# Performance work log

Hardware: AMD Instinct MI355X
Metric: run time of the kernel (lower is better)

Reference implementation:

```python
import jax, jax.numpy as jnp
import numpy as np

N_NODES = 50000
N_EDGES = 800000
IN_CH = 128
HID = 64
HEADS = 4
OUT_CH = 64
NEG_SLOPE = 0.2
EPS = 1e-16


def setup_inputs() -> dict:
    key = jax.random.key(0)
    ks = jax.random.split(key, 12)
    x = jax.random.normal(ks[0], (N_NODES, IN_CH), dtype=jnp.float32)
    edge_index = jax.random.randint(ks[1], (2, N_EDGES), 0, N_NODES, dtype=jnp.int32)
    s1 = 1.0 / np.sqrt(IN_CH)
    s2 = 1.0 / np.sqrt(HID * HEADS)
    s3 = 1.0 / np.sqrt(HID)
    return {
        "x": x,
        "edge_index": edge_index,
        # conv1: in -> heads*hid, concat=True
        "W1": jax.random.normal(ks[2], (IN_CH, HEADS * HID), dtype=jnp.float32) * s1,
        "a_src1": jax.random.normal(ks[3], (HEADS, HID), dtype=jnp.float32) * s3,
        "a_dst1": jax.random.normal(ks[4], (HEADS, HID), dtype=jnp.float32) * s3,
        "b1": jnp.zeros((HEADS * HID,), dtype=jnp.float32),
        # conv2: heads*hid -> hid, heads=1
        "W2": jax.random.normal(ks[5], (HEADS * HID, HID), dtype=jnp.float32) * s2,
        "a_src2": jax.random.normal(ks[6], (1, HID), dtype=jnp.float32) * s3,
        "a_dst2": jax.random.normal(ks[7], (1, HID), dtype=jnp.float32) * s3,
        "b2": jnp.zeros((HID,), dtype=jnp.float32),
        # final linear hid -> out
        "Wl": jax.random.normal(ks[8], (HID, OUT_CH), dtype=jnp.float32) * s3,
        "bl": jnp.zeros((OUT_CH,), dtype=jnp.float32),
    }


def _gat_conv(x, src, dst, W, a_src, a_dst, b, heads, ch):
    # x: [N, F]; src/dst: [E'] (self loops already appended)
    N = x.shape[0]
    h = (x @ W).reshape(N, heads, ch)                      # [N, H, C]
    alpha_src = jnp.einsum('nhc,hc->nh', h, a_src)         # [N, H]
    alpha_dst = jnp.einsum('nhc,hc->nh', h, a_dst)         # [N, H]
    e = jax.nn.leaky_relu(alpha_src[src] + alpha_dst[dst], NEG_SLOPE)  # [E, H]
    # per-destination segment softmax (every node has a self loop -> no empty segments)
    e_max = jax.ops.segment_max(e, dst, num_segments=N)
    e = jnp.exp(e - e_max[dst])
    denom = jax.ops.segment_sum(e, dst, num_segments=N)
    alpha = e / (denom[dst] + EPS)                         # [E, H]
    msg = h[src] * alpha[:, :, None]                       # [E, H, C]
    out = jax.ops.segment_sum(msg, dst, num_segments=N)    # [N, H, C]
    return out.reshape(N, heads * ch) + b


def reference(x, edge_index, W1, a_src1, a_dst1, b1, W2, a_src2, a_dst2, b2, Wl, bl):
    N = x.shape[0]
    loops = jnp.arange(N, dtype=edge_index.dtype)
    src = jnp.concatenate([edge_index[0], loops])
    dst = jnp.concatenate([edge_index[1], loops])
    h = _gat_conv(x, src, dst, W1, a_src1, a_dst1, b1, HEADS, HID)
    h = jax.nn.relu(h)
    h = _gat_conv(h, src, dst, W2, a_src2, a_dst2, b2, 1, HID)
    return h @ Wl + bl
```

## Files before the change

kernel.cpp:

```cpp
#include <hip/hip_runtime.h>

#define N_NODES 50000
#define N_EDGES 800000
#define E_TOT   850000
#define IN_CH   128
#define HID     64
#define HEADS   4
#define C1      256
#define OUT_CH  64
#define NEG_SLOPE 0.2f
#define EPSV    1e-16f

typedef _Float16 half_t;
typedef _Float16 half2_t __attribute__((ext_vector_type(2)));
typedef _Float16 half8_t __attribute__((ext_vector_type(8)));
typedef float f32x4 __attribute__((ext_vector_type(4)));

__device__ __forceinline__ float lrelu(float v) {
    return (v > 0.f) ? v : NEG_SLOPE * v;
}

__device__ __forceinline__ void acc8(float (&a)[8], float w, float4 r) {
    half2_t p;
    p = __builtin_bit_cast(half2_t, r.x); a[0] = fmaf(w, (float)p[0], a[0]); a[1] = fmaf(w, (float)p[1], a[1]);
    p = __builtin_bit_cast(half2_t, r.y); a[2] = fmaf(w, (float)p[0], a[2]); a[3] = fmaf(w, (float)p[1], a[3]);
    p = __builtin_bit_cast(half2_t, r.z); a[4] = fmaf(w, (float)p[0], a[4]); a[5] = fmaf(w, (float)p[1], a[5]);
    p = __builtin_bit_cast(half2_t, r.w); a[6] = fmaf(w, (float)p[0], a[6]); a[7] = fmaf(w, (float)p[1], a[7]);
}

#define NPREP ((IN_CH * C1 + C1 * HID + 255) / 256)
#define NCNT  ((E_TOT + 255) / 256)
__global__ __launch_bounds__(256) void k_count_prep(
    const int* __restrict__ ei, int* __restrict__ deg,
    const float* __restrict__ W1, const float* __restrict__ W2,
    half_t* __restrict__ W1T, half_t* __restrict__ W2T) {
    const int gb = blockIdx.x;
    const int tid = threadIdx.x;
    if (gb < NPREP) {
        int i = gb * 256 + tid;
        if (i < IN_CH * C1) {
            int c = i >> 7, k = i & 127;
            W1T[i] = (half_t)W1[k * C1 + c];
        }
        int j = i - IN_CH * C1;
        if (j >= 0 && j < C1 * HID) {
            int c = j >> 8, k = j & 255;
            W2T[j] = (half_t)W2[k * HID + c];
        }
    } else {
        int e = (gb - NPREP) * 256 + tid;
        if (e < E_TOT) {
            int d = (e < N_EDGES) ? ei[N_EDGES + e] : (e - N_EDGES);
            atomicAdd(&deg[d], 1);
        }
    }
}

#define SCAN_CH 1024
#define NB_SCAN ((N_NODES + SCAN_CH - 1) / SCAN_CH)

__global__ __launch_bounds__(256) void k_bsum(const int* __restrict__ deg,
                                              int* __restrict__ bsum) {
    const int b = blockIdx.x;
    const int tid = threadIdx.x;
    int sum = 0;
    for (int i = tid; i < SCAN_CH; i += 256) {
        int idx = b * SCAN_CH + i;
        sum += (idx < N_NODES) ? deg[idx] : 0;
    }
    #pragma unroll
    for (int d = 1; d < 64; d <<= 1) sum += __shfl_xor(sum, d, 64);
    __shared__ int ws[4];
    if ((tid & 63) == 0) ws[tid >> 6] = sum;
    __syncthreads();
    if (tid == 0) bsum[b] = ws[0] + ws[1] + ws[2] + ws[3];
}

__global__ __launch_bounds__(1024) void k_scanf(const int* __restrict__ deg,
                                                const int* __restrict__ bsum,
                                                int* __restrict__ rowptr,
                                                int* __restrict__ cursor) {
    __shared__ int wsum[16];
    __shared__ int boff_s;
    const int b = blockIdx.x;
    const int tid = threadIdx.x;
    const int lane = tid & 63;
    const int wv = tid >> 6;
    if (wv == 0) {
        int v = (lane < b) ? bsum[lane] : 0;
        #pragma unroll
        for (int d = 1; d < 64; d <<= 1) v += __shfl_xor(v, d, 64);
        if (lane == 0) boff_s = v;
    }
    if (b == 0 && tid == 0) rowptr[N_NODES] = E_TOT;
    const int i = b * SCAN_CH + tid;
    int v = (i < N_NODES) ? deg[i] : 0;
    int s = v;
    #pragma unroll
    for (int d = 1; d < 64; d <<= 1) {
        int t = __shfl_up(s, d, 64);
        if (lane >= d) s += t;
    }
    if (lane == 63) wsum[wv] = s;
    __syncthreads();
    if (wv == 0 && lane < 16) {
        int w = wsum[lane];
        #pragma unroll
        for (int d = 1; d < 16; d <<= 1) {
            int t = __shfl_up(w, d, 64);
            if (lane >= d) w += t;
        }
        wsum[lane] = w;
    }
    __syncthreads();
    int excl = boff_s + ((wv > 0) ? wsum[wv - 1] : 0) + (s - v);
    if (i < N_NODES) { rowptr[i] = excl; cursor[i] = excl; }
}

#define NSCAT ((E_TOT + 255) / 256)
#define NG1   ((N_NODES + 31) / 32)
#define XS1_LD 136
#define HS1_LD 264
__global__ __launch_bounds__(256) void k_scat_g1(
    const int* __restrict__ ei, int* __restrict__ cursor, int* __restrict__ csr_src,
    const float* __restrict__ x, const half_t* __restrict__ W1T,
    const float* __restrict__ a_s1, const float* __restrict__ a_d1,
    half_t* __restrict__ h1h, float* __restrict__ l1s, float* __restrict__ l1d) {
    __shared__ half_t xs[32 * XS1_LD];
    __shared__ half_t hs[32 * HS1_LD];
    const int tid = threadIdx.x;
    if (blockIdx.x < NSCAT) {
        int e = blockIdx.x * 256 + tid;
        if (e < E_TOT) {
            int s, d;
            if (e < N_EDGES) { s = ei[e]; d = ei[N_EDGES + e]; }
            else             { s = d = e - N_EDGES; }
            int pos = atomicAdd(&cursor[d], 1);
            csr_src[pos] = s;
        }
        return;
    }
    const int base = (blockIdx.x - NSCAT) * 32;
    const int rows = min(32, N_NODES - base);
    for (int idx = tid; idx < 32 * 16; idx += 256) {
        int row = idx >> 4, c8 = (idx & 15) * 8;
        half8_t hv = {0, 0, 0, 0, 0, 0, 0, 0};
        if (row < rows) {
            const float4 v0 = *(const float4*)(x + (size_t)(base + row) * IN_CH + c8);
            const float4 v1 = *(const float4*)(x + (size_t)(base + row) * IN_CH + c8 + 4);
            hv[0] = (half_t)v0.x; hv[1] = (half_t)v0.y; hv[2] = (half_t)v0.z; hv[3] = (half_t)v0.w;
            hv[4] = (half_t)v1.x; hv[5] = (half_t)v1.y; hv[6] = (half_t)v1.z; hv[7] = (half_t)v1.w;
        }
        *(half8_t*)(xs + row * XS1_LD + c8) = hv;
    }
    __syncthreads();
    const int lane = tid & 63;
    const int w = tid >> 6;
    const int cw = w * 64;
    const int lr = lane & 15;
    const int lg = lane >> 4;
    f32x4 acc[2][4];
    #pragma unroll
    for (int i = 0; i < 2; ++i)
        #pragma unroll
        for (int j = 0; j < 4; ++j)
            #pragma unroll
            for (int r = 0; r < 4; ++r) acc[i][j][r] = 0.f;

    #pragma unroll
    for (int kt = 0; kt < 4; ++kt) {
        const int k0 = kt * 32 + lg * 8;
        half8_t A0 = *(const half8_t*)(xs + lr * XS1_LD + k0);
        half8_t A1 = *(const half8_t*)(xs + (16 + lr) * XS1_LD + k0);
        #pragma unroll
        for (int ct = 0; ct < 4; ++ct) {
            half8_t B = *(const half8_t*)(W1T + (size_t)(cw + ct * 16 + lr) * IN_CH + k0);
            acc[0][ct] = __builtin_amdgcn_mfma_f32_16x16x32_f16(A0, B, acc[0][ct], 0, 0, 0);
            acc[1][ct] = __builtin_amdgcn_mfma_f32_16x16x32_f16(A1, B, acc[1][ct], 0, 0, 0);
        }
    }
    #pragma unroll
    for (int rt = 0; rt < 2; ++rt)
        #pragma unroll
        for (int ct = 0; ct < 4; ++ct)
            #pragma unroll
            for (int r = 0; r < 4; ++r)
                hs[(rt * 16 + lg * 4 + r) * HS1_LD + cw + ct * 16 + lr] = (half_t)acc[rt][ct][r];
    __syncthreads();
    for (int idx = tid; idx < 32 * 32; idx += 256) {
        int row = idx >> 5, c8 = (idx & 31) * 8;
        if (row < rows)
            *(float4*)(h1h + (size_t)(base + row) * C1 + c8) = *(const float4*)(hs + row * HS1_LD + c8);
    }
    {
        const int c4l = lane * 4;
        const float4 av = *(const float4*)(a_s1 + c4l);
        const float4 dv = *(const float4*)(a_d1 + c4l);
        #pragma unroll
        for (int i = 0; i < 8; ++i) {
            int row = w * 8 + i;
            if (row < rows) {
                float2 rr = *(const float2*)(hs + row * HS1_LD + c4l);
                half2_t ha = __builtin_bit_cast(half2_t, rr.x);
                half2_t hb = __builtin_bit_cast(half2_t, rr.y);
                float ps = (float)ha[0] * av.x + (float)ha[1] * av.y + (float)hb[0] * av.z + (float)hb[1] * av.w;
                float pd = (float)ha[0] * dv.x + (float)ha[1] * dv.y + (float)hb[0] * dv.z + (float)hb[1] * dv.w;
                #pragma unroll
                for (int d = 1; d < 16; d <<= 1) {
                    ps += __shfl_xor(ps, d, 64);
                    pd += __shfl_xor(pd, d, 64);
                }
                if ((lane & 15) == 0) {
                    int hh = lane >> 4;
                    l1s[(base + row) * HEADS + hh] = ps;
                    l1d[(base + row) * HEADS + hh] = pd;
                }
            }
        }
    }
}

__global__ __launch_bounds__(256) void k_agg1(
    const half_t* __restrict__ h1h, const float* __restrict__ l1s, const float* __restrict__ l1d,
    const int* __restrict__ rowptr, const int* __restrict__ csr_src,
    const float* __restrict__ b1, half_t* __restrict__ out1h) {
    const int tid = threadIdx.x;
    const int lane = tid & 63;
    const int wv = tid >> 6;
    const int n = blockIdx.x * 4 + wv;
    if (n >= N_NODES) return;
    const int beg = rowptr[n], end = rowptr[n + 1];
    const float4 ldv = *(const float4*)(l1d + (size_t)n * 4);
    const int half = lane >> 5;
    const int l32 = lane & 31;
    const int c8 = l32 * 8;
    const int hh = l32 >> 3;
    const float ldh = (hh & 2) ? ((hh & 1) ? ldv.w : ldv.z) : ((hh & 1) ? ldv.y : ldv.x);
    const float* l1sh = l1s + hh;
    const float4* hrows = (const float4*)h1h;
    float a[8] = {0.f, 0.f, 0.f, 0.f, 0.f, 0.f, 0.f, 0.f};
    float dn = 0.f;
    int e = beg + half;
    for (; e + 6 < end; e += 8) {
        int s0 = csr_src[e], s1 = csr_src[e + 2], s2 = csr_src[e + 4], s3 = csr_src[e + 6];
        float4 r0 = hrows[s0 * 32 + l32];
        float4 r1 = hrows[s1 * 32 + l32];
        float4 r2 = hrows[s2 * 32 + l32];
        float4 r3 = hrows[s3 * 32 + l32];
        float g0 = l1sh[s0 * 4] + ldh;
        float g1 = l1sh[s1 * 4] + ldh;
        float g2 = l1sh[s2 * 4] + ldh;
        float g3 = l1sh[s3 * 4] + ldh;
        float w0 = __expf(lrelu(g0));
        float w1 = __expf(lrelu(g1));
        float w2 = __expf(lrelu(g2));
        float w3 = __expf(lrelu(g3));
        dn += (w0 + w1) + (w2 + w3);
        acc8(a, w0, r0);
        acc8(a, w1, r1);
        acc8(a, w2, r2);
        acc8(a, w3, r3);
    }
    for (; e < end; e += 2) {
        int s0 = csr_src[e];
        float4 r0 = hrows[s0 * 32 + l32];
        float g0 = l1sh[s0 * 4] + ldh;
        float w0 = __expf(lrelu(g0));
        dn += w0;
        acc8(a, w0, r0);
    }
    #pragma unroll
    for (int j = 0; j < 8; ++j) a[j] += __shfl_xor(a[j], 32, 64);
    dn += __shfl_xor(dn, 32, 64);
    if (half == 0) {
        const float inv = 1.f / (dn + EPSV);
        const float4 bv0 = *(const float4*)(b1 + c8);
        const float4 bv1 = *(const float4*)(b1 + c8 + 4);
        half2_t p01, p23, p45, p67;
        p01[0] = (half_t)fmaxf(fmaf(a[0], inv, bv0.x), 0.f);
        p01[1] = (half_t)fmaxf(fmaf(a[1], inv, bv0.y), 0.f);
        p23[0] = (half_t)fmaxf(fmaf(a[2], inv, bv0.z), 0.f);
        p23[1] = (half_t)fmaxf(fmaf(a[3], inv, bv0.w), 0.f);
        p45[0] = (half_t)fmaxf(fmaf(a[4], inv, bv1.x), 0.f);
        p45[1] = (half_t)fmaxf(fmaf(a[5], inv, bv1.y), 0.f);
        p67[0] = (half_t)fmaxf(fmaf(a[6], inv, bv1.z), 0.f);
        p67[1] = (half_t)fmaxf(fmaf(a[7], inv, bv1.w), 0.f);
        float4 st;
        st.x = __builtin_bit_cast(float, p01);
        st.y = __builtin_bit_cast(float, p23);
        st.z = __builtin_bit_cast(float, p45);
        st.w = __builtin_bit_cast(float, p67);
        *(float4*)(out1h + (size_t)n * C1 + c8) = st;
    }
}

#define XS2_LD 264
#define HS2_LD 72
__global__ __launch_bounds__(256) void k_gemm2(
    const half_t* __restrict__ out1h, const half_t* __restrict__ W2T,
    const float* __restrict__ a_s2, const float* __restrict__ a_d2,
    half_t* __restrict__ h2h, float* __restrict__ l2s, float* __restrict__ l2d) {
    __shared__ half_t xs[32 * XS2_LD];
    __shared__ half_t hs[32 * HS2_LD];
    const int base = blockIdx.x * 32;
    const int rows = min(32, N_NODES - base);
    const int tid = threadIdx.x;
    for (int idx = tid; idx < 32 * 32; idx += 256) {
        int row = idx >> 5, c8 = (idx & 31) * 8;
        half8_t hv = {0, 0, 0, 0, 0, 0, 0, 0};
        if (row < rows) hv = *(const half8_t*)(out1h + (size_t)(base + row) * C1 + c8);
        *(half8_t*)(xs + row * XS2_LD + c8) = hv;
    }
    __syncthreads();
    const int lane = tid & 63;
    const int w = tid >> 6;
    const int lr = lane & 15;
    const int lg = lane >> 4;
    f32x4 acc0, acc1;
    #pragma unroll
    for (int r = 0; r < 4; ++r) { acc0[r] = 0.f; acc1[r] = 0.f; }
    #pragma unroll
    for (int kt = 0; kt < 8; ++kt) {
        const int k0 = kt * 32 + lg * 8;
        half8_t A0 = *(const half8_t*)(xs + lr * XS2_LD + k0);
        half8_t A1 = *(const half8_t*)(xs + (16 + lr) * XS2_LD + k0);
        half8_t B  = *(const half8_t*)(W2T + (size_t)(w * 16 + lr) * C1 + k0);
        acc0 = __builtin_amdgcn_mfma_f32_16x16x32_f16(A0, B, acc0, 0, 0, 0);
        acc1 = __builtin_amdgcn_mfma_f32_16x16x32_f16(A1, B, acc1, 0, 0, 0);
    }
    #pragma unroll
    for (int r = 0; r < 4; ++r) {
        hs[(lg * 4 + r) * HS2_LD + w * 16 + lr] = (half_t)acc0[r];
        hs[(16 + lg * 4 + r) * HS2_LD + w * 16 + lr] = (half_t)acc1[r];
    }
    __syncthreads();
    {
        int idx = tid;
        int row = idx >> 3, c8 = (idx & 7) * 8;
        if (row < rows)
            *(float4*)(h2h + (size_t)(base + row) * HID + c8) = *(const float4*)(hs + row * HS2_LD + c8);
    }
    {
        const float vas = a_s2[lane];
        const float vad = a_d2[lane];
        #pragma unroll
        for (int i = 0; i < 8; ++i) {
            int row = w * 8 + i;
            if (row < rows) {
                float v = (float)hs[row * HS2_LD + lane];
                float ps = v * vas, pd = v * vad;
                #pragma unroll
                for (int d = 1; d < 64; d <<= 1) {
                    ps += __shfl_xor(ps, d, 64);
                    pd += __shfl_xor(pd, d, 64);
                }
                if (lane == 0) { l2s[base + row] = ps; l2d[base + row] = pd; }
            }
        }
    }
}

__global__ __launch_bounds__(256) void k_agg2(
    const half_t* __restrict__ h2h, const float* __restrict__ l2s, const float* __restrict__ l2d,
    const int* __restrict__ rowptr, const int* __restrict__ csr_src,
    const float* __restrict__ b2, const float* __restrict__ Wl, const float* __restrict__ bl,
    float* __restrict__ out) {
    __shared__ float Wls[HID * OUT_CH];
    __shared__ float vsh[4][HID];
    const int tid = threadIdx.x;
    const int lane = tid & 63;
    const int wv = tid >> 6;
    for (int i = tid; i < HID * OUT_CH; i += 256) Wls[i] = Wl[i];
    const int n = blockIdx.x * 4 + wv;
    const bool active = (n < N_NODES);
    if (active) {
        const int beg = rowptr[n], end = rowptr[n + 1];
        const float ld = l2d[n];
        const int q = lane >> 4;
        const int l16 = lane & 15;
        const float2* h2rows = (const float2*)h2h;
        float a0 = 0.f, a1 = 0.f, a2 = 0.f, a3 = 0.f, dn = 0.f;
        int e = beg + q;
        for (; e + 12 < end; e += 16) {
            int s0 = csr_src[e], s1 = csr_src[e + 4], s2 = csr_src[e + 8], s3 = csr_src[e + 12];
            float2 v0 = h2rows[s0 * 16 + l16];
            float2 v1 = h2rows[s1 * 16 + l16];
            float2 v2 = h2rows[s2 * 16 + l16];
            float2 v3 = h2rows[s3 * 16 + l16];
            float g0 = l2s[s0] + ld;
            float g1 = l2s[s1] + ld;
            float g2 = l2s[s2] + ld;
            float g3 = l2s[s3] + ld;
            float w0 = __expf(lrelu(g0));
            float w1 = __expf(lrelu(g1));
            float w2 = __expf(lrelu(g2));
            float w3 = __expf(lrelu(g3));
            dn += (w0 + w1) + (w2 + w3);
            half2_t p;
            p = __builtin_bit_cast(half2_t, v0.x); a0 = fmaf(w0, (float)p[0], a0); a1 = fmaf(w0, (float)p[1], a1);
            p = __builtin_bit_cast(half2_t, v0.y); a2 = fmaf(w0, (float)p[0], a2); a3 = fmaf(w0, (float)p[1], a3);
            p = __builtin_bit_cast(half2_t, v1.x); a0 = fmaf(w1, (float)p[0], a0); a1 = fmaf(w1, (float)p[1], a1);
            p = __builtin_bit_cast(half2_t, v1.y); a2 = fmaf(w1, (float)p[0], a2); a3 = fmaf(w1, (float)p[1], a3);
            p = __builtin_bit_cast(half2_t, v2.x); a0 = fmaf(w2, (float)p[0], a0); a1 = fmaf(w2, (float)p[1], a1);
            p = __builtin_bit_cast(half2_t, v2.y); a2 = fmaf(w2, (float)p[0], a2); a3 = fmaf(w2, (float)p[1], a3);
            p = __builtin_bit_cast(half2_t, v3.x); a0 = fmaf(w3, (float)p[0], a0); a1 = fmaf(w3, (float)p[1], a1);
            p = __builtin_bit_cast(half2_t, v3.y); a2 = fmaf(w3, (float)p[0], a2); a3 = fmaf(w3, (float)p[1], a3);
        }
        for (; e < end; e += 4) {
            int s = csr_src[e];
            float2 v = h2rows[s * 16 + l16];
            float lg = l2s[s] + ld;
            float w = __expf(lrelu(lg));
            dn += w;
            half2_t p;
            p = __builtin_bit_cast(half2_t, v.x); a0 = fmaf(w, (float)p[0], a0); a1 = fmaf(w, (float)p[1], a1);
            p = __builtin_bit_cast(half2_t, v.y); a2 = fmaf(w, (float)p[0], a2); a3 = fmaf(w, (float)p[1], a3);
        }
        a0 += __shfl_xor(a0, 16, 64); a0 += __shfl_xor(a0, 32, 64);
        a1 += __shfl_xor(a1, 16, 64); a1 += __shfl_xor(a1, 32, 64);
        a2 += __shfl_xor(a2, 16, 64); a2 += __shfl_xor(a2, 32, 64);
        a3 += __shfl_xor(a3, 16, 64); a3 += __shfl_xor(a3, 32, 64);
        dn += __shfl_xor(dn, 16, 64); dn += __shfl_xor(dn, 32, 64);
        if (q == 0) {
            const float inv = 1.f / (dn + EPSV);
            const float4 bv = *(const float4*)(b2 + l16 * 4);
            float4 vv;
            vv.x = fmaf(a0, inv, bv.x);
            vv.y = fmaf(a1, inv, bv.y);
            vv.z = fmaf(a2, inv, bv.z);
            vv.w = fmaf(a3, inv, bv.w);
            *(float4*)(&vsh[wv][l16 * 4]) = vv;
        }
    }
    __syncthreads();
    if (active) {
        float o = bl[lane];
        #pragma unroll
        for (int c2 = 0; c2 < HID; ++c2)
            o = fmaf(vsh[wv][c2], Wls[c2 * OUT_CH + lane], o);
        out[(size_t)n * OUT_CH + lane] = o;
    }
}

extern "C" void kernel_launch(void* const* d_in, const int* in_sizes, int n_in,
                              void* d_out, int out_size, void* d_ws, size_t ws_size,
                              hipStream_t stream) {
    const float* x   = (const float*)d_in[0];
    const int*   ei  = (const int*)d_in[1];
    const float* W1  = (const float*)d_in[2];
    const float* as1 = (const float*)d_in[3];
    const float* ad1 = (const float*)d_in[4];
    const float* b1  = (const float*)d_in[5];
    const float* W2  = (const float*)d_in[6];
    const float* as2 = (const float*)d_in[7];
    const float* ad2 = (const float*)d_in[8];
    const float* b2  = (const float*)d_in[9];
    const float* Wl  = (const float*)d_in[10];
    const float* bl  = (const float*)d_in[11];
    float* out = (float*)d_out;

    char* p = (char*)d_ws;
    auto alloc = [&](size_t bytes) {
        char* r = p;
        p += (bytes + 255) & ~(size_t)255;
        return r;
    };
    int* deg      = (int*)alloc((size_t)N_NODES * 4);
    int* rowptr   = (int*)alloc((size_t)(N_NODES + 1) * 4);
    int* cursor   = (int*)alloc((size_t)N_NODES * 4);
    int* csr_src  = (int*)alloc((size_t)E_TOT * 4);
    int* bsum     = (int*)alloc(64 * 4);
    half_t* W1T   = (half_t*)alloc((size_t)IN_CH * C1 * 2);
    half_t* W2T   = (half_t*)alloc((size_t)C1 * HID * 2);
    half_t* h1h   = (half_t*)alloc((size_t)N_NODES * C1 * 2);
    float* l1s    = (float*)alloc((size_t)N_NODES * HEADS * 4);
    float* l1d    = (float*)alloc((size_t)N_NODES * HEADS * 4);
    half_t* out1h = (half_t*)alloc((size_t)N_NODES * C1 * 2);
    half_t* h2h   = (half_t*)alloc((size_t)N_NODES * HID * 2);
    float* l2s    = (float*)alloc((size_t)N_NODES * 4);
    float* l2d    = (float*)alloc((size_t)N_NODES * 4);

    (void)hipMemsetAsync(deg, 0, (size_t)N_NODES * 4, stream);
    k_count_prep<<<NPREP + NCNT, 256, 0, stream>>>(ei, deg, W1, W2, W1T, W2T);
    k_bsum<<<NB_SCAN, 256, 0, stream>>>(deg, bsum);
    k_scanf<<<NB_SCAN, 1024, 0, stream>>>(deg, bsum, rowptr, cursor);
    k_scat_g1<<<NSCAT + NG1, 256, 0, stream>>>(ei, cursor, csr_src,
                                               x, W1T, as1, ad1, h1h, l1s, l1d);
    k_agg1<<<(N_NODES + 3) / 4, 256, 0, stream>>>(h1h, l1s, l1d, rowptr, csr_src, b1, out1h);
    k_gemm2<<<(N_NODES + 31) / 32, 256, 0, stream>>>(out1h, W2T, as2, ad2, h2h, l2s, l2d);
    k_agg2<<<(N_NODES + 3) / 4, 256, 0, stream>>>(h2h, l2s, l2d, rowptr, csr_src, b2, Wl, bl, out);
}
```

Measured before the change: 259.0 us.

## Record per-edge rank during degree count to scatter CSR without atomics

The degree-counting atomicAdd now saves its return value as a per-edge rank, so the CSR scatter computes each slot as rowptr[d]+rank and needs no second atomic pass on a cursor array. The scatter is split out of the fused scatter+GEMM1 kernel into its own launch, and GEMM1 becomes a standalone kernel. This removes 850K contended atomics but adds an extra 3.4MB erank write and read plus one more kernel launch, and it gives up the overlap between scatter and GEMM1 blocks.

```diff
diff --git a/kernel.cpp b/kernel.cpp
--- a/kernel.cpp
+++ b/kernel.cpp
@@ -31,7 +31,7 @@
 #define NPREP ((IN_CH * C1 + C1 * HID + 255) / 256)
 #define NCNT  ((E_TOT + 255) / 256)
 __global__ __launch_bounds__(256) void k_count_prep(
-    const int* __restrict__ ei, int* __restrict__ deg,
+    const int* __restrict__ ei, int* __restrict__ deg, int* __restrict__ erank,
     const float* __restrict__ W1, const float* __restrict__ W2,
     half_t* __restrict__ W1T, half_t* __restrict__ W2T) {
     const int gb = blockIdx.x;
@@ -51,7 +51,7 @@
         int e = (gb - NPREP) * 256 + tid;
         if (e < E_TOT) {
             int d = (e < N_EDGES) ? ei[N_EDGES + e] : (e - N_EDGES);
-            atomicAdd(&deg[d], 1);
+            erank[e] = atomicAdd(&deg[d], 1);
         }
     }
 }
@@ -78,8 +78,7 @@
 
 __global__ __launch_bounds__(1024) void k_scanf(const int* __restrict__ deg,
                                                 const int* __restrict__ bsum,
-                                                int* __restrict__ rowptr,
-                                                int* __restrict__ cursor) {
+                                                int* __restrict__ rowptr) {
     __shared__ int wsum[16];
     __shared__ int boff_s;
     const int b = blockIdx.x;
@@ -114,34 +113,30 @@
     }
     __syncthreads();
     int excl = boff_s + ((wv > 0) ? wsum[wv - 1] : 0) + (s - v);
-    if (i < N_NODES) { rowptr[i] = excl; cursor[i] = excl; }
-}
-
-#define NSCAT ((E_TOT + 255) / 256)
-#define NG1   ((N_NODES + 31) / 32)
+    if (i < N_NODES) rowptr[i] = excl;
+}
+
+__global__ void k_scatter(const int* __restrict__ ei, const int* __restrict__ erank,
+                          const int* __restrict__ rowptr, int* __restrict__ csr_src) {
+    int e = blockIdx.x * blockDim.x + threadIdx.x;
+    if (e >= E_TOT) return;
+    int s, d;
+    if (e < N_EDGES) { s = ei[e]; d = ei[N_EDGES + e]; }
+    else             { s = d = e - N_EDGES; }
+    csr_src[rowptr[d] + erank[e]] = s;
+}
+
 #define XS1_LD 136
 #define HS1_LD 264
-__global__ __launch_bounds__(256) void k_scat_g1(
-    const int* __restrict__ ei, int* __restrict__ cursor, int* __restrict__ csr_src,
+__global__ __launch_bounds__(256) void k_gemm1(
     const float* __restrict__ x, const half_t* __restrict__ W1T,
     const float* __restrict__ a_s1, const float* __restrict__ a_d1,
     half_t* __restrict__ h1h, float* __restrict__ l1s, float* __restrict__ l1d) {
     __shared__ half_t xs[32 * XS1_LD];
     __shared__ half_t hs[32 * HS1_LD];
-    const int tid = threadIdx.x;
-    if (blockIdx.x < NSCAT) {
-        int e = blockIdx.x * 256 + tid;
-        if (e < E_TOT) {
-            int s, d;
-            if (e < N_EDGES) { s = ei[e]; d = ei[N_EDGES + e]; }
-            else             { s = d = e - N_EDGES; }
-            int pos = atomicAdd(&cursor[d], 1);
-            csr_src[pos] = s;
-        }
-        return;
-    }
-    const int base = (blockIdx.x - NSCAT) * 32;
+    const int base = blockIdx.x * 32;
     const int rows = min(32, N_NODES - base);
+    const int tid = threadIdx.x;
     for (int idx = tid; idx < 32 * 16; idx += 256) {
         int row = idx >> 4, c8 = (idx & 15) * 8;
         half8_t hv = {0, 0, 0, 0, 0, 0, 0, 0};
@@ -467,7 +462,7 @@
     };
     int* deg      = (int*)alloc((size_t)N_NODES * 4);
     int* rowptr   = (int*)alloc((size_t)(N_NODES + 1) * 4);
-    int* cursor   = (int*)alloc((size_t)N_NODES * 4);
+    int* erank    = (int*)alloc((size_t)E_TOT * 4);
     int* csr_src  = (int*)alloc((size_t)E_TOT * 4);
     int* bsum     = (int*)alloc(64 * 4);
     half_t* W1T   = (half_t*)alloc((size_t)IN_CH * C1 * 2);
@@ -481,11 +476,11 @@
     float* l2d    = (float*)alloc((size_t)N_NODES * 4);
 
     (void)hipMemsetAsync(deg, 0, (size_t)N_NODES * 4, stream);
-    k_count_prep<<<NPREP + NCNT, 256, 0, stream>>>(ei, deg, W1, W2, W1T, W2T);
+    k_count_prep<<<NPREP + NCNT, 256, 0, stream>>>(ei, deg, erank, W1, W2, W1T, W2T);
     k_bsum<<<NB_SCAN, 256, 0, stream>>>(deg, bsum);
-    k_scanf<<<NB_SCAN, 1024, 0, stream>>>(deg, bsum, rowptr, cursor);
-    k_scat_g1<<<NSCAT + NG1, 256, 0, stream>>>(ei, cursor, csr_src,
-                                               x, W1T, as1, ad1, h1h, l1s, l1d);
+    k_scanf<<<NB_SCAN, 1024, 0, stream>>>(deg, bsum, rowptr);
+    k_scatter<<<(E_TOT + 255) / 256, 256, 0, stream>>>(ei, erank, rowptr, csr_src);
+    k_gemm1<<<(N_NODES + 31) / 32, 256, 0, stream>>>(x, W1T, as1, ad1, h1h, l1s, l1d);
     k_agg1<<<(N_NODES + 3) / 4, 256, 0, stream>>>(h1h, l1s, l1d, rowptr, csr_src, b1, out1h);
     k_gemm2<<<(N_NODES + 31) / 32, 256, 0, stream>>>(out1h, W2T, as2, ad2, h2h, l2s, l2d);
     k_agg2<<<(N_NODES + 3) / 4, 256, 0, stream>>>(h2h, l2s, l2d, rowptr, csr_src, b2, Wl, bl, out);
```

Result: faster. 226.5 us (-12.6%).
